# Kernel tuning notes

Hardware: AMD Instinct MI355X
Metric: run time of the kernel (lower is better)

Reference implementation:

```python
import jax, jax.numpy as jnp
import numpy as np
import math

D_MODEL = 1024
H = 16
D_K = D_MODEL // H
SEQ = 4096
NEG = -1000000000.0  # mask constant from the original code


def setup_inputs() -> dict:
    key = jax.random.key(0)
    ks = jax.random.split(key, 7)
    return {
        "Q": jax.random.normal(ks[0], (SEQ, D_MODEL), dtype=jnp.float32),
        "K": jax.random.normal(ks[1], (SEQ, D_MODEL), dtype=jnp.float32),
        "V": jax.random.normal(ks[2], (SEQ, D_MODEL), dtype=jnp.float32),
        "W_Q": jax.random.normal(ks[3], (H, D_MODEL, D_K), dtype=jnp.float32),
        "W_K": jax.random.normal(ks[4], (H, D_MODEL, D_K), dtype=jnp.float32),
        "W_V": jax.random.normal(ks[5], (H, D_MODEL, D_K), dtype=jnp.float32),
        "W_O": jax.random.normal(ks[6], (D_MODEL, D_MODEL), dtype=jnp.float32),
        "mask": 1,
    }


def reference(Q, K, V, W_Q, W_K, W_V, W_O, mask):
    d_k = W_Q.shape[-1]
    s = Q.shape[0]
    # batched per-head projections: [h, s, d_k]
    Qh = jnp.einsum("sd,hdk->hsk", Q, W_Q)
    Kh = jnp.einsum("sd,hdk->hsk", K, W_K)
    Vh = jnp.einsum("sd,hdk->hsk", V, W_V)
    # scores: [h, s_q, s_k]
    scores = jnp.einsum("hqk,hsk->hqs", Qh, Kh) / math.sqrt(d_k)
    if mask:
        # faithful to torch: tril(scores) + triu(ones, 1) * -1e9
        lower = jnp.tril(jnp.ones((s, s), dtype=scores.dtype))
        upper = jnp.triu(jnp.ones((s, s), dtype=scores.dtype), k=1)
        scores = scores * lower + upper * NEG
    attn = jax.nn.softmax(scores, axis=-1)
    heads = jnp.einsum("hqs,hsk->hqk", attn, Vh)  # [h, s, d_k]
    # concat heads along feature dim in head order -> [s, h*d_k]
    concat = jnp.transpose(heads, (1, 0, 2)).reshape(s, -1)
    return concat @ W_O
```

## Files before the change

### kernel.cpp

```cpp
#include <hip/hip_runtime.h>
#include <hip/hip_bf16.h>

constexpr int S      = 4096;
constexpr int DMODEL = 1024;
constexpr int H      = 16;
constexpr int DK     = 64;

typedef __attribute__((ext_vector_type(8))) short          short8;
typedef __attribute__((ext_vector_type(4))) short          short4v;
typedef __attribute__((ext_vector_type(4))) float          float4v;
typedef __attribute__((ext_vector_type(4))) unsigned short ushort4v;
typedef __attribute__((ext_vector_type(8))) unsigned short ushort8;

__device__ __forceinline__ unsigned short f2bf(float x) {
    unsigned u = __builtin_bit_cast(unsigned, x);
    u += 0x7FFFu + ((u >> 16) & 1u);
    return (unsigned short)(u >> 16);
}
__device__ __forceinline__ float bf2f(unsigned short h) {
    unsigned u = ((unsigned)h) << 16;
    return __builtin_bit_cast(float, u);
}

__global__ __launch_bounds__(256) void split_inputs(const float* __restrict__ Q,
                                                    const float* __restrict__ K,
                                                    const float* __restrict__ V,
                                                    unsigned short* __restrict__ QH,
                                                    unsigned short* __restrict__ QL,
                                                    unsigned short* __restrict__ KH,
                                                    unsigned short* __restrict__ KL,
                                                    unsigned short* __restrict__ Vb)
{
    const int z = blockIdx.z;
    const size_t base = ((size_t)blockIdx.x * 256 + threadIdx.x) * 8;
    const float* src = (z == 0) ? Q : (z == 1) ? K : V;
    const float4 a = *(const float4*)(src + base);
    const float4 b = *(const float4*)(src + base + 4);
    const float xs[8] = {a.x, a.y, a.z, a.w, b.x, b.y, b.z, b.w};
    ushort8 hv, lv;
#pragma unroll
    for (int j = 0; j < 8; ++j) {
        const unsigned short h = f2bf(xs[j]);
        hv[j] = h;
        lv[j] = f2bf(xs[j] - bf2f(h));
    }
    if (z == 0)      { *(ushort8*)(QH + base) = hv; *(ushort8*)(QL + base) = lv; }
    else if (z == 1) { *(ushort8*)(KH + base) = hv; *(ushort8*)(KL + base) = lv; }
    else             { *(ushort8*)(Vb + base) = hv; }
}

__global__ __launch_bounds__(256) void transpose_w(const float* __restrict__ in,
                                                   unsigned short* __restrict__ oh,
                                                   unsigned short* __restrict__ ol,
                                                   int z_mult, int rstride)
{
    __shared__ float Ts[64][65];
    const int t  = threadIdx.x;
    const int z  = blockIdx.z;
    const int r0 = blockIdx.x * 64;
    const float* src = in + (size_t)z * z_mult;
#pragma unroll
    for (int i = 0; i < 4; ++i) {
        const int row = (t >> 4) + i * 16;
        const int col = (t & 15) * 4;
        const float4 v = *(const float4*)&src[(size_t)(r0 + row) * rstride + col];
        Ts[row][col + 0] = v.x; Ts[row][col + 1] = v.y;
        Ts[row][col + 2] = v.z; Ts[row][col + 3] = v.w;
    }
    __syncthreads();
#pragma unroll
    for (int i = 0; i < 4; ++i) {
        const int c  = (t >> 4) + i * 16;
        const int rb = (t & 15) * 4;
        ushort4v hv, lv;
#pragma unroll
        for (int j = 0; j < 4; ++j) {
            const float x = Ts[rb + j][c];
            const unsigned short h = f2bf(x);
            hv[j] = h;
            lv[j] = f2bf(x - bf2f(h));
        }
        const size_t o = (size_t)(z * 64 + c) * 1024 + r0 + rb;
        *(ushort4v*)&oh[o] = hv;
        if (ol) *(ushort4v*)&ol[o] = lv;
    }
}

template <bool SPLIT>
__device__ __forceinline__ void gemm_core(unsigned short* __restrict__ sm,
                                          const unsigned short* __restrict__ Ah,
                                          const unsigned short* __restrict__ Al,
                                          const unsigned short* __restrict__ Bh,
                                          const unsigned short* __restrict__ Bl,
                                          float* __restrict__ C,
                                          int m0, int n0)
{
    unsigned short* AsH = sm;
    unsigned short* BsH = sm + 4096;
    unsigned short* AsL = sm + 8192;
    unsigned short* BsL = sm + 12288;

    const int t    = threadIdx.x;
    const int wave = t >> 6;
    const int lane = t & 63;
    const int quad = lane >> 4;
    const int l15  = lane & 15;
    const int wm   = (wave & 1) * 64;
    const int wn   = (wave >> 1) * 64;

    float4v acc[4][4];
#pragma unroll
    for (int mi = 0; mi < 4; ++mi)
#pragma unroll
        for (int ni = 0; ni < 4; ++ni)
#pragma unroll
            for (int r = 0; r < 4; ++r) acc[mi][ni][r] = 0.f;

    for (int k0 = 0; k0 < 1024; k0 += 32) {
        __syncthreads();
#pragma unroll
        for (int i = 0; i < 2; ++i) {
            const int c   = t + 256 * i;
            const int row = c >> 2;
            const int kc  = (c & 3) * 8;
            *(ushort8*)&AsH[row * 32 + kc] =
                *(const ushort8*)&Ah[(size_t)(m0 + row) * 1024 + k0 + kc];
            *(ushort8*)&BsH[row * 32 + kc] =
                *(const ushort8*)&Bh[(size_t)(n0 + row) * 1024 + k0 + kc];
            if (SPLIT) {
                *(ushort8*)&AsL[row * 32 + kc] =
                    *(const ushort8*)&Al[(size_t)(m0 + row) * 1024 + k0 + kc];
                *(ushort8*)&BsL[row * 32 + kc] =
                    *(const ushort8*)&Bl[(size_t)(n0 + row) * 1024 + k0 + kc];
            }
        }
        __syncthreads();

        short8 afh[4], bfh[4], afl[4], bfl[4];
#pragma unroll
        for (int mi = 0; mi < 4; ++mi)
            afh[mi] = *(const short8*)&AsH[(wm + mi * 16 + l15) * 32 + quad * 8];
#pragma unroll
        for (int ni = 0; ni < 4; ++ni)
            bfh[ni] = *(const short8*)&BsH[(wn + ni * 16 + l15) * 32 + quad * 8];
        if (SPLIT) {
#pragma unroll
            for (int mi = 0; mi < 4; ++mi)
                afl[mi] = *(const short8*)&AsL[(wm + mi * 16 + l15) * 32 + quad * 8];
#pragma unroll
            for (int ni = 0; ni < 4; ++ni)
                bfl[ni] = *(const short8*)&BsL[(wn + ni * 16 + l15) * 32 + quad * 8];
        }

#pragma unroll
        for (int mi = 0; mi < 4; ++mi)
#pragma unroll
            for (int ni = 0; ni < 4; ++ni) {
                acc[mi][ni] = __builtin_amdgcn_mfma_f32_16x16x32_bf16(
                    afh[mi], bfh[ni], acc[mi][ni], 0, 0, 0);
                if (SPLIT) {
                    acc[mi][ni] = __builtin_amdgcn_mfma_f32_16x16x32_bf16(
                        afh[mi], bfl[ni], acc[mi][ni], 0, 0, 0);
                    acc[mi][ni] = __builtin_amdgcn_mfma_f32_16x16x32_bf16(
                        afl[mi], bfh[ni], acc[mi][ni], 0, 0, 0);
                }
            }
    }

#pragma unroll
    for (int mi = 0; mi < 4; ++mi)
#pragma unroll
        for (int r = 0; r < 4; ++r) {
            const int m = m0 + wm + mi * 16 + quad * 4 + r;
            float* cp = C + (size_t)m * 1024 + n0 + wn + l15;
#pragma unroll
            for (int ni = 0; ni < 4; ++ni) cp[ni * 16] = acc[mi][ni][r];
        }
}

__global__ __launch_bounds__(256) void proj_mfma(
    const unsigned short* __restrict__ XqH, const unsigned short* __restrict__ XqL,
    const unsigned short* __restrict__ XkH, const unsigned short* __restrict__ XkL,
    const unsigned short* __restrict__ Xv,
    const unsigned short* __restrict__ WqtH, const unsigned short* __restrict__ WqtL,
    const unsigned short* __restrict__ WktH, const unsigned short* __restrict__ WktL,
    const unsigned short* __restrict__ Wvt,
    float* __restrict__ Qc, float* __restrict__ Kc, float* __restrict__ Vc)
{
    __shared__ __align__(16) unsigned short smem[4 * 4096];
    const int m0 = blockIdx.x * 128, n0 = blockIdx.y * 128;
    if (blockIdx.z == 0)
        gemm_core<true>(smem, XqH, XqL, WqtH, WqtL, Qc, m0, n0);
    else if (blockIdx.z == 1)
        gemm_core<true>(smem, XkH, XkL, WktH, WktL, Kc, m0, n0);
    else
        gemm_core<false>(smem, Xv, nullptr, Wvt, nullptr, Vc, m0, n0);
}

__global__ __launch_bounds__(256) void out_gemm_mfma(
    const unsigned short* __restrict__ Ocb,
    const unsigned short* __restrict__ WOt,
    float* __restrict__ out)
{
    __shared__ __align__(16) unsigned short smem[2 * 4096];
    gemm_core<false>(smem, Ocb, nullptr, WOt, nullptr, out,
                     blockIdx.x * 128, blockIdx.y * 128);
}

__global__ __launch_bounds__(256) void attn_mfma(const float* __restrict__ Qc,
                                                 const float* __restrict__ Kc,
                                                 const float* __restrict__ Vc,
                                                 unsigned short* __restrict__ Ocb)
{
    __shared__ __align__(16) short Khi[64][72];
    __shared__ __align__(16) short Klo[64][72];
    __shared__ __align__(16) short Vts[64][72];
    __shared__ __align__(16) short Pb[4][16][72];

    const int bid = blockIdx.x;
    const int h   = bid & 15;
    const int qt  = 63 - (bid >> 4);
    const int q0  = qt * 64;

    const int t    = threadIdx.x;
    const int wave = t >> 6;
    const int lane = t & 63;
    const int quad = lane >> 4;
    const int l15  = lane & 15;

    short8 qhi[2], qlo[2];
    {
        const int qrow = q0 + wave * 16 + l15;
        const float* qp = Qc + (size_t)qrow * DMODEL + h * 64 + quad * 8;
#pragma unroll
        for (int ks = 0; ks < 2; ++ks) {
            float4 a = *(const float4*)(qp + ks * 32);
            float4 b = *(const float4*)(qp + ks * 32 + 4);
            const float xs[8] = {a.x, a.y, a.z, a.w, b.x, b.y, b.z, b.w};
#pragma unroll
            for (int j = 0; j < 8; ++j) {
                const unsigned short hi = f2bf(xs[j]);
                const unsigned short lo = f2bf(xs[j] - bf2f(hi));
                qhi[ks][j] = (short)hi;
                qlo[ks][j] = (short)lo;
            }
        }
    }

    float m_r[4] = {-1e30f, -1e30f, -1e30f, -1e30f};
    float l_r[4] = {0.f, 0.f, 0.f, 0.f};
    float4v oacc[4];
#pragma unroll
    for (int nt = 0; nt < 4; ++nt)
#pragma unroll
        for (int r = 0; r < 4; ++r) oacc[nt][r] = 0.f;

    const int sr  = t >> 2;
    const int sc0 = (t & 3) * 16;

    for (int jt = 0; jt <= qt; ++jt) {
        const int j0 = jt * 64;
        const float* kp = Kc + (size_t)(j0 + sr) * DMODEL + h * 64 + sc0;
        const float* vp = Vc + (size_t)(j0 + sr) * DMODEL + h * 64 + sc0;
#pragma unroll
        for (int ch = 0; ch < 4; ++ch) {
            const float4 f = *(const float4*)(kp + ch * 4);
            const float xs[4] = {f.x, f.y, f.z, f.w};
            short4v hv, lv;
#pragma unroll
            for (int j = 0; j < 4; ++j) {
                const unsigned short hi = f2bf(xs[j]);
                const unsigned short lo = f2bf(xs[j] - bf2f(hi));
                hv[j] = (short)hi;
                lv[j] = (short)lo;
            }
            *(short4v*)&Khi[sr][sc0 + ch * 4] = hv;
            *(short4v*)&Klo[sr][sc0 + ch * 4] = lv;
            const float4 g = *(const float4*)(vp + ch * 4);
            Vts[sc0 + ch * 4 + 0][sr] = (short)f2bf(g.x);
            Vts[sc0 + ch * 4 + 1][sr] = (short)f2bf(g.y);
            Vts[sc0 + ch * 4 + 2][sr] = (short)f2bf(g.z);
            Vts[sc0 + ch * 4 + 3][sr] = (short)f2bf(g.w);
        }
        __syncthreads();

        float4v sacc[4];
#pragma unroll
        for (int nt = 0; nt < 4; ++nt)
#pragma unroll
            for (int r = 0; r < 4; ++r) sacc[nt][r] = 0.f;
#pragma unroll
        for (int nt = 0; nt < 4; ++nt) {
            const int key = nt * 16 + l15;
#pragma unroll
            for (int ks = 0; ks < 2; ++ks) {
                const short8 bh = *(const short8*)&Khi[key][ks * 32 + quad * 8];
                const short8 bl = *(const short8*)&Klo[key][ks * 32 + quad * 8];
                sacc[nt] = __builtin_amdgcn_mfma_f32_16x16x32_bf16(qhi[ks], bh, sacc[nt], 0, 0, 0);
                sacc[nt] = __builtin_amdgcn_mfma_f32_16x16x32_bf16(qhi[ks], bl, sacc[nt], 0, 0, 0);
                sacc[nt] = __builtin_amdgcn_mfma_f32_16x16x32_bf16(qlo[ks], bh, sacc[nt], 0, 0, 0);
            }
        }

#pragma unroll
        for (int nt = 0; nt < 4; ++nt) {
            const int jg = j0 + nt * 16 + l15;
#pragma unroll
            for (int r = 0; r < 4; ++r) {
                const int qg = q0 + wave * 16 + quad * 4 + r;
                const float v = sacc[nt][r] * 0.125f;
                sacc[nt][r] = (jg > qg) ? -1e9f : v;
            }
        }

        float rmax[4];
#pragma unroll
        for (int r = 0; r < 4; ++r)
            rmax[r] = fmaxf(fmaxf(sacc[0][r], sacc[1][r]), fmaxf(sacc[2][r], sacc[3][r]));
#pragma unroll
        for (int off = 1; off < 16; off <<= 1)
#pragma unroll
            for (int r = 0; r < 4; ++r)
                rmax[r] = fmaxf(rmax[r], __shfl_xor(rmax[r], off));

        float alpha[4];
#pragma unroll
        for (int r = 0; r < 4; ++r) {
            const float mn = fmaxf(m_r[r], rmax[r]);
            alpha[r] = __expf(m_r[r] - mn);
            m_r[r] = mn;
        }

        float rsum[4] = {0.f, 0.f, 0.f, 0.f};
#pragma unroll
        for (int nt = 0; nt < 4; ++nt)
#pragma unroll
            for (int r = 0; r < 4; ++r) {
                const float p = __expf(sacc[nt][r] - m_r[r]);
                sacc[nt][r] = p;
                rsum[r] += p;
            }
#pragma unroll
        for (int off = 1; off < 16; off <<= 1)
#pragma unroll
            for (int r = 0; r < 4; ++r)
                rsum[r] += __shfl_xor(rsum[r], off);
#pragma unroll
        for (int r = 0; r < 4; ++r)
            l_r[r] = l_r[r] * alpha[r] + rsum[r];

#pragma unroll
        for (int nt = 0; nt < 4; ++nt)
#pragma unroll
            for (int r = 0; r < 4; ++r)
                oacc[nt][r] *= alpha[r];

#pragma unroll
        for (int nt = 0; nt < 4; ++nt)
#pragma unroll
            for (int r = 0; r < 4; ++r)
                Pb[wave][quad * 4 + r][nt * 16 + l15] = (short)f2bf(sacc[nt][r]);
        __asm__ volatile("s_waitcnt lgkmcnt(0)" ::: "memory");

        short8 af[2];
        af[0] = *(const short8*)&Pb[wave][l15][quad * 8];
        af[1] = *(const short8*)&Pb[wave][l15][32 + quad * 8];
#pragma unroll
        for (int nt = 0; nt < 4; ++nt) {
            const int dk = nt * 16 + l15;
#pragma unroll
            for (int ks = 0; ks < 2; ++ks) {
                const short8 bv = *(const short8*)&Vts[dk][ks * 32 + quad * 8];
                oacc[nt] = __builtin_amdgcn_mfma_f32_16x16x32_bf16(af[ks], bv, oacc[nt], 0, 0, 0);
            }
        }
        __syncthreads();
    }

#pragma unroll
    for (int r = 0; r < 4; ++r) {
        const float inv = 1.0f / l_r[r];
        const int qg = q0 + wave * 16 + quad * 4 + r;
        unsigned short* op = Ocb + (size_t)qg * DMODEL + h * 64 + l15;
#pragma unroll
        for (int nt = 0; nt < 4; ++nt)
            op[nt * 16] = f2bf(oacc[nt][r] * inv);
    }
}

extern "C" void kernel_launch(void* const* d_in, const int* in_sizes, int n_in,
                              void* d_out, int out_size, void* d_ws, size_t ws_size,
                              hipStream_t stream)
{
    const float* Q  = (const float*)d_in[0];
    const float* K  = (const float*)d_in[1];
    const float* V  = (const float*)d_in[2];
    const float* WQ = (const float*)d_in[3];
    const float* WK = (const float*)d_in[4];
    const float* WV = (const float*)d_in[5];
    const float* WO = (const float*)d_in[6];

    float* out = (float*)d_out;

    const size_t SD4 = (size_t)S * DMODEL * 4;
    const size_t SD2 = (size_t)S * DMODEL * 2;
    const size_t W2  = (size_t)DMODEL * DMODEL * 2;
    char* p = (char*)d_ws;
    auto take = [&](size_t b) { char* r = p; p += b; return r; };

    float* Qc = (float*)take(SD4);
    float* Kc = (float*)take(SD4);
    float* Vc = (float*)take(SD4);
    unsigned short* XqH = (unsigned short*)take(SD2);
    unsigned short* XqL = (unsigned short*)take(SD2);
    unsigned short* XkH = (unsigned short*)take(SD2);
    unsigned short* XkL = (unsigned short*)take(SD2);
    unsigned short* Xv  = (unsigned short*)take(SD2);
    unsigned short* WqtH = (unsigned short*)take(W2);
    unsigned short* WqtL = (unsigned short*)take(W2);
    unsigned short* WktH = (unsigned short*)take(W2);
    unsigned short* WktL = (unsigned short*)take(W2);
    unsigned short* Wvt  = (unsigned short*)take(W2);
    unsigned short* WOt  = (unsigned short*)take(W2);
    unsigned short* Ocb  = (unsigned short*)take(SD2);

    split_inputs<<<dim3(2048, 1, 3), 256, 0, stream>>>(Q, K, V,
                                                       XqH, XqL, XkH, XkL, Xv);
    transpose_w<<<dim3(16, 1, 16), 256, 0, stream>>>(WQ, WqtH, WqtL, 65536, 64);
    transpose_w<<<dim3(16, 1, 16), 256, 0, stream>>>(WK, WktH, WktL, 65536, 64);
    transpose_w<<<dim3(16, 1, 16), 256, 0, stream>>>(WV, Wvt, nullptr, 65536, 64);
    transpose_w<<<dim3(16, 1, 16), 256, 0, stream>>>(WO, WOt, nullptr, 64, 1024);
    proj_mfma<<<dim3(S / 128, DMODEL / 128, 3), 256, 0, stream>>>(
        XqH, XqL, XkH, XkL, Xv, WqtH, WqtL, WktH, WktL, Wvt, Qc, Kc, Vc);
    attn_mfma<<<dim3((S / 64) * H), 256, 0, stream>>>(Qc, Kc, Vc, Ocb);
    out_gemm_mfma<<<dim3(S / 128, DMODEL / 128), 256, 0, stream>>>(Ocb, WOt, out);
}
```

Measured before the change: 406.1 us.

## Enlarge attention query tile to 128 rows and register-prefetch next K/V tile

The attention kernel now runs 8 waves per block over 128 query rows. Each K/V tile staged in shared memory is therefore reused by twice as many queries, which halves global K/V traffic and conversion work per query. The next tile's K/V floats are loaded into registers after the barrier so the loads overlap the MFMA compute. The cost is fewer blocks (512) with a coarser causal imbalance. The diagonal tiles also do more masked work, and register pressure rises under the 512-thread bound.

New measurement: 431.3 us. 6.2% more time.

```diff
diff --git a/kernel.cpp b/kernel.cpp
--- a/kernel.cpp
+++ b/kernel.cpp
@@ -207,7 +207,7 @@
                      blockIdx.x * 128, blockIdx.y * 128);
 }
 
-__global__ __launch_bounds__(256) void attn_mfma(const float* __restrict__ Qc,
+__global__ __launch_bounds__(512) void attn_mfma(const float* __restrict__ Qc,
                                                  const float* __restrict__ Kc,
                                                  const float* __restrict__ Vc,
                                                  unsigned short* __restrict__ Ocb)
@@ -215,12 +215,13 @@
     __shared__ __align__(16) short Khi[64][72];
     __shared__ __align__(16) short Klo[64][72];
     __shared__ __align__(16) short Vts[64][72];
-    __shared__ __align__(16) short Pb[4][16][72];
-
-    const int bid = blockIdx.x;
-    const int h   = bid & 15;
-    const int qt  = 63 - (bid >> 4);
-    const int q0  = qt * 64;
+    __shared__ __align__(16) short Pb[8][16][72];
+
+    const int bid  = blockIdx.x;
+    const int h    = bid & 15;
+    const int qt   = 31 - (bid >> 4);
+    const int q0   = qt * 128;
+    const int jmax = 2 * qt + 1;
 
     const int t    = threadIdx.x;
     const int wave = t >> 6;
@@ -255,34 +256,46 @@
 #pragma unroll
         for (int r = 0; r < 4; ++r) oacc[nt][r] = 0.f;
 
-    const int sr  = t >> 2;
-    const int sc0 = (t & 3) * 16;
-
-    for (int jt = 0; jt <= qt; ++jt) {
+    const int sr  = t >> 3;
+    const int sc0 = (t & 7) * 8;
+
+    float4 kpre[2], vpre[2];
+    {
+        const float* kp = Kc + (size_t)sr * DMODEL + h * 64 + sc0;
+        const float* vp = Vc + (size_t)sr * DMODEL + h * 64 + sc0;
+        kpre[0] = *(const float4*)kp;  kpre[1] = *(const float4*)(kp + 4);
+        vpre[0] = *(const float4*)vp;  vpre[1] = *(const float4*)(vp + 4);
+    }
+
+    for (int jt = 0; jt <= jmax; ++jt) {
         const int j0 = jt * 64;
-        const float* kp = Kc + (size_t)(j0 + sr) * DMODEL + h * 64 + sc0;
-        const float* vp = Vc + (size_t)(j0 + sr) * DMODEL + h * 64 + sc0;
-#pragma unroll
-        for (int ch = 0; ch < 4; ++ch) {
-            const float4 f = *(const float4*)(kp + ch * 4);
-            const float xs[4] = {f.x, f.y, f.z, f.w};
+#pragma unroll
+        for (int c = 0; c < 2; ++c) {
+            const float xs[4] = {kpre[c].x, kpre[c].y, kpre[c].z, kpre[c].w};
             short4v hv, lv;
 #pragma unroll
             for (int j = 0; j < 4; ++j) {
                 const unsigned short hi = f2bf(xs[j]);
-                const unsigned short lo = f2bf(xs[j] - bf2f(hi));
                 hv[j] = (short)hi;
-                lv[j] = (short)lo;
-            }
-            *(short4v*)&Khi[sr][sc0 + ch * 4] = hv;
-            *(short4v*)&Klo[sr][sc0 + ch * 4] = lv;
-            const float4 g = *(const float4*)(vp + ch * 4);
-            Vts[sc0 + ch * 4 + 0][sr] = (short)f2bf(g.x);
-            Vts[sc0 + ch * 4 + 1][sr] = (short)f2bf(g.y);
-            Vts[sc0 + ch * 4 + 2][sr] = (short)f2bf(g.z);
-            Vts[sc0 + ch * 4 + 3][sr] = (short)f2bf(g.w);
+                lv[j] = (short)f2bf(xs[j] - bf2f(hi));
+            }
+            *(short4v*)&Khi[sr][sc0 + c * 4] = hv;
+            *(short4v*)&Klo[sr][sc0 + c * 4] = lv;
+            const float ys[4] = {vpre[c].x, vpre[c].y, vpre[c].z, vpre[c].w};
+            Vts[sc0 + c * 4 + 0][sr] = (short)f2bf(ys[0]);
+            Vts[sc0 + c * 4 + 1][sr] = (short)f2bf(ys[1]);
+            Vts[sc0 + c * 4 + 2][sr] = (short)f2bf(ys[2]);
+            Vts[sc0 + c * 4 + 3][sr] = (short)f2bf(ys[3]);
         }
         __syncthreads();
+
+        if (jt < jmax) {
+            const int jn = j0 + 64;
+            const float* kp = Kc + (size_t)(jn + sr) * DMODEL + h * 64 + sc0;
+            const float* vp = Vc + (size_t)(jn + sr) * DMODEL + h * 64 + sc0;
+            kpre[0] = *(const float4*)kp;  kpre[1] = *(const float4*)(kp + 4);
+            vpre[0] = *(const float4*)vp;  vpre[1] = *(const float4*)(vp + 4);
+        }
 
         float4v sacc[4];
 #pragma unroll
@@ -432,6 +445,6 @@
     transpose_w<<<dim3(16, 1, 16), 256, 0, stream>>>(WO, WOt, nullptr, 64, 1024);
     proj_mfma<<<dim3(S / 128, DMODEL / 128, 3), 256, 0, stream>>>(
         XqH, XqL, XkH, XkL, Xv, WqtH, WqtL, WktH, WktL, Wvt, Qc, Kc, Vc);
-    attn_mfma<<<dim3((S / 64) * H), 256, 0, stream>>>(Qc, Kc, Vc, Ocb);
+    attn_mfma<<<dim3((S / 128) * H), 512, 0, stream>>>(Qc, Kc, Vc, Ocb);
     out_gemm_mfma<<<dim3(S / 128, DMODEL / 128), 256, 0, stream>>>(Ocb, WOt, out);
 }
```
